# Optimization experiments

Hardware: AMD Instinct MI355X
Metric: run time of the kernel (lower is better)

## Reference

```python
import jax, jax.numpy as jnp
import numpy as np

# Dims (match init_kwargs): d_model=1024, H=16 heads, hd=64, lift=2 -> Nlift=128, top-k t=32
B, T, D = 1, 2048, 1024
H, HD, LIFT, TK = 16, 64, 2, 32
N = LIFT * HD  # 128 lifted dims per head
EPS = 1e-12


def topk_sparsify(x, k):
    """ReLU then keep only the top-k values per last-dim row (rest zeroed).
    Mathematically identical to the torch COO top-k construction: the sparse
    matrix equals the dense matrix with non-top-k entries zeroed."""
    x = jax.nn.relu(x)
    vals, idx = jax.lax.top_k(x, k)              # (..., k)
    n = x.shape[-1]
    flat_idx = idx.reshape(-1, k)
    flat_vals = vals.reshape(-1, k)
    R = flat_idx.shape[0]
    out = jnp.zeros((R, n), dtype=x.dtype)
    out = out.at[jnp.arange(R)[:, None], flat_idx].set(flat_vals)
    return out.reshape(x.shape)


def setup_inputs() -> dict:
    key = jax.random.key(0)
    ks = jax.random.split(key, 6)
    x = jax.random.normal(ks[0], (B, T, D), jnp.float32)
    W_q = jax.random.normal(ks[1], (H * N, D), jnp.float32) * 0.02
    W_k = jax.random.normal(ks[2], (H * N, D), jnp.float32) * 0.02
    W_v = jax.random.normal(ks[3], (H * HD, D), jnp.float32) * 0.02
    W_o = jax.random.normal(ks[4], (D, H * HD), jnp.float32) * 0.02
    sink = jax.random.normal(ks[5], (H, HD), jnp.float32) * 0.02
    log_beta = jnp.zeros((), jnp.float32)
    return {"x": x, "W_q": W_q, "W_k": W_k, "W_v": W_v, "W_o": W_o,
            "sink": sink, "log_beta": log_beta}


def reference(x, W_q, W_k, W_v, W_o, sink, log_beta):
    # Projections (Linear with no bias: x @ W.T)
    q = (x @ W_q.T).reshape(B, T, H, N)
    k = (x @ W_k.T).reshape(B, T, H, N)
    v = (x @ W_v.T).reshape(B, T, H, HD)

    # ReLU + top-k sparsification of lifted Q/K rows
    qs = topk_sparsify(q, TK).transpose(0, 2, 1, 3)  # (B,H,T,N)
    kk = topk_sparsify(k, TK).transpose(0, 2, 1, 3)  # (B,H,T,N)

    # A = Qs @ Ks^T per (batch, head) block; spspmm only produces same-block
    # entries, so the per-head batched matmul is the exact dense equivalent.
    A = jnp.einsum('bhin,bhjn->bhij', qs, kk)        # (B,H,T,T), all >= 0

    # Causal filter: keep j <= i
    causal = jnp.tril(jnp.ones((T, T), dtype=bool))
    A = jnp.where(causal, A, jnp.zeros((), A.dtype))

    # p=1 normalization with learned sink mass beta
    denom = A.sum(-1)                                # (B,H,T)
    beta = jnp.exp(log_beta)
    denom_ws = denom + beta
    A = A / jnp.maximum(denom_ws, EPS)[..., None]

    vh = v.transpose(0, 2, 1, 3)                     # (B,H,T,HD)
    Y = jnp.einsum('bhij,bhjd->bhid', A, vh)         # (B,H,T,HD)
    Y = Y + (beta / denom_ws)[..., None] * sink[None, :, None, :]

    Y = Y.transpose(0, 2, 1, 3).reshape(B, T, H * HD)
    return Y @ W_o.T
```

## Files before the change

### kernel.cpp

```cpp
#include <hip/hip_runtime.h>

typedef __attribute__((ext_vector_type(8))) short bf8v;
typedef __attribute__((ext_vector_type(4))) float f4v;
typedef unsigned short u16;
typedef unsigned int   u32;
#define AS1 __attribute__((address_space(1)))
#define AS3 __attribute__((address_space(3)))

__device__ inline u16 f2b(float f){
  u32 u = __builtin_bit_cast(u32, f);
  u += 0x7fffu + ((u >> 16) & 1u);
  return (u16)(u >> 16);
}

__global__ __launch_bounds__(256) void conv_all(const float* __restrict__ x,  const float* __restrict__ wq,
                                                const float* __restrict__ wk, const float* __restrict__ wv,
                                                const float* __restrict__ wo,
                                                u16* xb, u16* wqb, u16* wkb, u16* wvb, u16* wob){
  int i = blockIdx.x * 256 + threadIdx.x;
  const float* src; u16* dst; int off;
  if      (i <  524288){ src = x;  dst = xb;  off = i; }
  else if (i < 1048576){ src = wq; dst = wqb; off = i -  524288; }
  else if (i < 1572864){ src = wk; dst = wkb; off = i - 1048576; }
  else if (i < 1835008){ src = wv; dst = wvb; off = i - 1572864; }
  else                 { src = wo; dst = wob; off = i - 1835008; }
  float4 v = ((const float4*)src)[off];
  uint2 r;
  r.x = (u32)f2b(v.x) | ((u32)f2b(v.y) << 16);
  r.y = (u32)f2b(v.z) | ((u32)f2b(v.w) << 16);
  ((uint2*)dst)[off] = r;
}

template<int NFR>
__device__ __forceinline__ void gemm_core(const u16* __restrict__ A, const u16* __restrict__ B,
                                          int K, int m0, int n0, u16* lds, f4v (&acc)[4][NFR]){
  const int tid = threadIdx.x;
  const int l = tid & 63, w = tid >> 6;
  const int wrow = (w >> 1) * 64, wcol = (w & 1) * (NFR * 16);
  constexpr int SB = 8192 + NFR * 2048;
  #pragma unroll
  for (int a = 0; a < 4; a++)
    #pragma unroll
    for (int b = 0; b < NFR; b++) acc[a][b] = (f4v)0.0f;

  const int crow = l >> 3;
  const int ksrc = ((l & 7) ^ crow) * 8;

  auto stage = [&](int k0, int buf){
    const u16* Ab = A + (size_t)m0 * K + k0;
    const u16* Bb = B + (size_t)n0 * K + k0;
    u16* At = lds + buf * SB;
    u16* Bt = At + 8192;
    #pragma unroll
    for (int c = 0; c < 4; c++){
      int chunk = w * 4 + c;
      int row = chunk * 8 + crow;
      __builtin_amdgcn_global_load_lds((const AS1 void*)(Ab + (size_t)row * K + ksrc),
                                       (AS3 void*)(At + chunk * 512), 16, 0, 0);
    }
    if constexpr (NFR == 4){
      #pragma unroll
      for (int c = 0; c < 4; c++){
        int chunk = w * 4 + c;
        int row = chunk * 8 + crow;
        __builtin_amdgcn_global_load_lds((const AS1 void*)(Bb + (size_t)row * K + ksrc),
                                         (AS3 void*)(Bt + chunk * 512), 16, 0, 0);
      }
    } else {
      #pragma unroll
      for (int c = 0; c < 2; c++){
        int chunk = w * 2 + c;
        int row = chunk * 8 + crow;
        __builtin_amdgcn_global_load_lds((const AS1 void*)(Bb + (size_t)row * K + ksrc),
                                         (AS3 void*)(Bt + chunk * 512), 16, 0, 0);
      }
    }
  };

  stage(0, 0);
  __syncthreads();
  int buf = 0;
  for (int k0 = 0; k0 < K; k0 += 64){
    if (k0 + 64 < K) stage(k0 + 64, buf ^ 1);
    const u16* At = lds + buf * SB;
    const u16* Bt = At + 8192;
    #pragma unroll
    for (int kk = 0; kk < 2; kk++){
      bf8v af[4], bfr[NFR];
      #pragma unroll
      for (int mr = 0; mr < 4; mr++){
        int row = wrow + mr * 16 + (l & 15);
        af[mr] = *(const bf8v*)(At + row * 64 + (((kk * 32 + (l >> 4) * 8)) ^ ((row & 7) * 8)));
      }
      #pragma unroll
      for (int nc = 0; nc < NFR; nc++){
        int row = wcol + nc * 16 + (l & 15);
        bfr[nc] = *(const bf8v*)(Bt + row * 64 + (((kk * 32 + (l >> 4) * 8)) ^ ((row & 7) * 8)));
      }
      #pragma unroll
      for (int mr = 0; mr < 4; mr++)
        #pragma unroll
        for (int nc = 0; nc < NFR; nc++)
          acc[mr][nc] = __builtin_amdgcn_mfma_f32_16x16x32_bf16(af[mr], bfr[nc], acc[mr][nc], 0, 0, 0);
    }
    __syncthreads();
    buf ^= 1;
  }
}

__global__ __launch_bounds__(256) void qkv_gemm(const u16* __restrict__ xb,
                                                const u16* __restrict__ wqb, const u16* __restrict__ wkb,
                                                const u16* __restrict__ wvb,
                                                u16* qf, u16* kf, u16* vtb){
  __shared__ u16 lds[32768];
  int b = (blockIdx.x & 7) * 80 + (blockIdx.x >> 3);
  const u16* Bp; int which;
  if (b < 256)      { Bp = wqb; which = 0; }
  else if (b < 512) { Bp = wkb; which = 1; b -= 256; }
  else              { Bp = wvb; which = 2; b -= 512; }
  int sh = (which == 2) ? 3 : 4;
  int m0 = (b >> sh) * 128, n0 = (b & ((1 << sh) - 1)) * 128;

  f4v acc[4][4];
  gemm_core<4>(xb, Bp, 1024, m0, n0, lds, acc);

  const int l = threadIdx.x & 63, w = threadIdx.x >> 6;
  const int wrow = (w >> 1) * 64, wcol = (w & 1) * 64;
  if (which < 2){
    u16* C = which ? kf : qf;
    #pragma unroll
    for (int mr = 0; mr < 4; mr++)
      #pragma unroll
      for (int nc = 0; nc < 4; nc++)
        #pragma unroll
        for (int rr = 0; rr < 4; rr++){
          int row = m0 + wrow + mr * 16 + (l >> 4) * 4 + rr;
          int col = n0 + wcol + nc * 16 + (l & 15);
          C[(size_t)row * 2048 + col] = f2b(acc[mr][nc][rr]);
        }
  } else {
    #pragma unroll
    for (int mr = 0; mr < 4; mr++)
      #pragma unroll
      for (int nc = 0; nc < 4; nc++){
        int gcol = n0 + wcol + nc * 16 + (l & 15);
        int t0 = m0 + wrow + mr * 16 + (l >> 4) * 4;
        uint2 pk;
        pk.x = (u32)f2b(acc[mr][nc][0]) | ((u32)f2b(acc[mr][nc][1]) << 16);
        pk.y = (u32)f2b(acc[mr][nc][2]) | ((u32)f2b(acc[mr][nc][3]) << 16);
        *(uint2*)(vtb + (size_t)gcol * 2048 + t0) = pk;
      }
  }
}

__global__ __launch_bounds__(256) void o_gemm(const u16* __restrict__ yb, const u16* __restrict__ wob,
                                              float* out){
  __shared__ u16 lds[24576];
  int b = (blockIdx.x & 7) * 32 + (blockIdx.x >> 3);
  int m0 = (b >> 4) * 128, n0 = (b & 15) * 64;
  f4v acc[4][2];
  gemm_core<2>(yb, wob, 1024, m0, n0, lds, acc);
  const int l = threadIdx.x & 63, w = threadIdx.x >> 6;
  const int wrow = (w >> 1) * 64, wcol = (w & 1) * 32;
  #pragma unroll
  for (int mr = 0; mr < 4; mr++)
    #pragma unroll
    for (int nc = 0; nc < 2; nc++)
      #pragma unroll
      for (int rr = 0; rr < 4; rr++){
        int row = m0 + wrow + mr * 16 + (l >> 4) * 4 + rr;
        int col = n0 + wcol + nc * 16 + (l & 15);
        out[(size_t)row * 1024 + col] = acc[mr][nc][rr];
      }
}

__global__ __launch_bounds__(256) void topk2(const u16* __restrict__ qf, const u16* __restrict__ kf,
                                             u16* __restrict__ qsb, u16* __restrict__ ksb){
  int w = threadIdx.x >> 6, l = threadIdx.x & 63;
  int b = blockIdx.x;
  const u16* src; u16* dst;
  if (b < 2048){ src = qf; dst = qsb; } else { src = kf; dst = ksb; b -= 2048; }
  int base = b * 16 + w * 4;
  u32 u0[4], u1[4], pre[4];
  int tt[4], hh[4];
  #pragma unroll
  for (int j = 0; j < 4; j++){
    int r = base + j;
    tt[j] = r >> 4; hh[j] = r & 15;
    u32 pair = ((const u32*)(src + (size_t)tt[j] * 2048 + hh[j] * 128))[l];
    u0[j] = pair & 0xFFFFu; u1[j] = pair >> 16;
    if (u0[j] & 0x8000u) u0[j] = 0;
    if (u1[j] & 0x8000u) u1[j] = 0;
    pre[j] = 0;
  }
  for (int bb = 14; bb >= 0; --bb){
    #pragma unroll
    for (int j = 0; j < 4; j++){
      u32 cand = pre[j] | (1u << bb);
      int c = __builtin_popcountll(__ballot(u0[j] >= cand)) + __builtin_popcountll(__ballot(u1[j] >= cand));
      if (c >= 32) pre[j] = cand;
    }
  }
  #pragma unroll
  for (int j = 0; j < 4; j++){
    u32 o0 = (u0[j] >= pre[j]) ? u0[j] : 0u;
    u32 o1 = (u1[j] >= pre[j]) ? u1[j] : 0u;
    ((u32*)(dst + ((size_t)hh[j] * 2048 + tt[j]) * 128))[l] = o0 | (o1 << 16);
  }
}

__global__ __launch_bounds__(512) void attn3(const u16* __restrict__ qs, const u16* __restrict__ ks,
                                             const u16* __restrict__ vt, const float* __restrict__ sink,
                                             const float* __restrict__ logbeta, u16* __restrict__ yout,
                                             float* __restrict__ Yp, float* __restrict__ Dp){
  __shared__ u16 Kt[2][8192];
  __shared__ u16 Vt[2][4096];
  __shared__ u16 St[8][16 * 72];
  const int tid = threadIdx.x, l = tid & 63, w = tid >> 6;
  const int b = blockIdx.x;
  const int slot = b >> 3;
  const int h = (b & 7) + 8 * (slot / 40);
  const int u = slot % 40;
  int it, chunk, nch;
  if (u < 4)       { it = u; chunk = 0; nch = 1; }
  else if (u < 12) { it = 4 + ((u - 4) >> 1);  chunk = (u - 4) & 1;  nch = 2; }
  else if (u < 24) { it = 8 + (u - 12) / 3;    chunk = (u - 12) % 3; nch = 3; }
  else             { it = 12 + ((u - 24) >> 2); chunk = (u - 24) & 3; nch = 4; }
  const int tiles = 2 * it + 2;
  const int jt0 = (tiles * chunk) / nch;
  const int jt1 = (tiles * (chunk + 1)) / nch;
  const int qrow0 = it * 128 + w * 16;
  const float beta = expf(logbeta[0]);

  bf8v qfr[4];
  {
    int trow = qrow0 + (l & 15);
    const u16* qrow = qs + ((size_t)h * 2048 + trow) * 128 + (l >> 4) * 8;
    #pragma unroll
    for (int kk = 0; kk < 4; kk++) qfr[kk] = *(const bf8v*)(qrow + kk * 32);
  }

  f4v accY[4];
  #pragma unroll
  for (int c = 0; c < 4; c++) accY[c] = (f4v)0.0f;
  float dsum[4] = {0.f, 0.f, 0.f, 0.f};

  const u16* kroot = ks + (size_t)h * 2048 * 128;
  const u16* vroot = vt + (size_t)h * 64 * 2048;

  auto stage = [&](int jt, int buf){
    const u16* kbase = kroot + (size_t)jt * 64 * 128;
    #pragma unroll
    for (int i = 0; i < 2; i++){
      int g = i * 512 + tid;
      int r = g >> 4, c = g & 15;
      __builtin_amdgcn_global_load_lds((const AS1 void*)(kbase + r * 128 + (c ^ (r & 7)) * 8),
                                       (AS3 void*)(&Kt[buf][(i * 512 + w * 64) * 8]), 16, 0, 0);
    }
    {
      int d = tid >> 3, c = tid & 7;
      __builtin_amdgcn_global_load_lds((const AS1 void*)(vroot + (size_t)d * 2048 + jt * 64 + (c ^ (d & 7)) * 8),
                                       (AS3 void*)(&Vt[buf][w * 512]), 16, 0, 0);
    }
  };

  stage(jt0, 0);
  __syncthreads();
  int buf = 0;
  for (int jt = jt0; jt < jt1; ++jt){
    if (jt + 1 < jt1) stage(jt + 1, buf ^ 1);

    if (jt * 64 <= qrow0 + 15){
      f4v accS[4];
      #pragma unroll
      for (int c = 0; c < 4; c++) accS[c] = (f4v)0.0f;
      __builtin_amdgcn_s_setprio(1);
      #pragma unroll
      for (int c = 0; c < 4; c++){
        int r = c * 16 + (l & 15);
        #pragma unroll
        for (int kk = 0; kk < 4; kk++){
          int ch = kk * 4 + (l >> 4);
          bf8v kfr = *(const bf8v*)(&Kt[buf][r * 128 + ((ch ^ (r & 7)) * 8)]);
          accS[c] = __builtin_amdgcn_mfma_f32_16x16x32_bf16(qfr[kk], kfr, accS[c], 0, 0, 0);
        }
      }
      __builtin_amdgcn_s_setprio(0);
      if (jt * 64 + 63 > qrow0){
        #pragma unroll
        for (int c = 0; c < 4; c++)
          #pragma unroll
          for (int rr = 0; rr < 4; rr++){
            int i = qrow0 + (l >> 4) * 4 + rr;
            int j = jt * 64 + c * 16 + (l & 15);
            if (j > i) accS[c][rr] = 0.f;
          }
      }
      #pragma unroll
      for (int c = 0; c < 4; c++)
        #pragma unroll
        for (int rr = 0; rr < 4; rr++){
          dsum[rr] += accS[c][rr];
          St[w][((l >> 4) * 4 + rr) * 72 + c * 16 + (l & 15)] = f2b(accS[c][rr]);
        }
      __builtin_amdgcn_s_setprio(1);
      #pragma unroll
      for (int k2 = 0; k2 < 2; k2++){
        bf8v afr = *(const bf8v*)(&St[w][(l & 15) * 72 + k2 * 32 + (l >> 4) * 8]);
        #pragma unroll
        for (int c = 0; c < 4; c++){
          int d = c * 16 + (l & 15);
          int ch = k2 * 4 + (l >> 4);
          bf8v vfr = *(const bf8v*)(&Vt[buf][d * 64 + ((ch ^ (d & 7)) * 8)]);
          accY[c] = __builtin_amdgcn_mfma_f32_16x16x32_bf16(afr, vfr, accY[c], 0, 0, 0);
        }
      }
      __builtin_amdgcn_s_setprio(0);
    }
    __syncthreads();
    buf ^= 1;
  }

  #pragma unroll
  for (int rr = 0; rr < 4; rr++){
    float s = dsum[rr];
    s += __shfl_xor(s, 1, 64);
    s += __shfl_xor(s, 2, 64);
    s += __shfl_xor(s, 4, 64);
    s += __shfl_xor(s, 8, 64);
    dsum[rr] = s;
  }

  if (nch == 1){
    #pragma unroll
    for (int c = 0; c < 4; c++){
      float sv = sink[h * 64 + c * 16 + (l & 15)];
      #pragma unroll
      for (int rr = 0; rr < 4; rr++){
        float den = dsum[rr] + beta;
        float inv = 1.0f / fmaxf(den, 1e-12f);
        float y = (accY[c][rr] + beta * sv) * inv;
        int row = qrow0 + (l >> 4) * 4 + rr;
        yout[(size_t)row * 1024 + h * 64 + c * 16 + (l & 15)] = f2b(y);
      }
    }
  } else {
    float* yp = Yp + ((size_t)h * 40 + u) * 8192;
    #pragma unroll
    for (int c = 0; c < 4; c++)
      #pragma unroll
      for (int rr = 0; rr < 4; rr++){
        int rowib = w * 16 + (l >> 4) * 4 + rr;
        yp[rowib * 64 + c * 16 + (l & 15)] = accY[c][rr];
      }
    if ((l & 15) == 0){
      #pragma unroll
      for (int rr = 0; rr < 4; rr++)
        Dp[((size_t)h * 40 + u) * 128 + w * 16 + (l >> 4) * 4 + rr] = dsum[rr];
    }
  }
}

__global__ __launch_bounds__(256) void attn_reduce(const float* __restrict__ Yp, const float* __restrict__ Dp,
                                                   const float* __restrict__ sink, const float* __restrict__ logbeta,
                                                   u16* __restrict__ yout){
  int blk = blockIdx.x;
  int h = blk / 12, it = 4 + blk % 12;
  int nch = it / 4 + 1;
  int u0 = (it < 8) ? 4 + (it - 4) * 2 : (it < 12) ? 12 + (it - 8) * 3 : 24 + (it - 12) * 4;
  float beta = expf(logbeta[0]);
  __shared__ float inv_s[128];
  int t = threadIdx.x;
  if (t < 128){
    float s = 0.f;
    for (int c = 0; c < nch; c++) s += Dp[((size_t)h * 40 + u0 + c) * 128 + t];
    inv_s[t] = 1.0f / fmaxf(s + beta, 1e-12f);
  }
  __syncthreads();
  const float* base = Yp + ((size_t)h * 40 + u0) * 8192;
  #pragma unroll
  for (int e = 0; e < 32; e++){
    int idx = e * 256 + t;
    float acc = 0.f;
    for (int c = 0; c < nch; c++) acc += base[c * 8192 + idx];
    int row = idx >> 6, col = idx & 63;
    float y = (acc + beta * sink[h * 64 + col]) * inv_s[row];
    yout[(size_t)(it * 128 + row) * 1024 + h * 64 + col] = f2b(y);
  }
}

extern "C" void kernel_launch(void* const* d_in, const int* in_sizes, int n_in,
                              void* d_out, int out_size, void* d_ws, size_t ws_size,
                              hipStream_t stream){
  const float* x    = (const float*)d_in[0];
  const float* Wq   = (const float*)d_in[1];
  const float* Wk   = (const float*)d_in[2];
  const float* Wv   = (const float*)d_in[3];
  const float* Wo   = (const float*)d_in[4];
  const float* sink = (const float*)d_in[5];
  const float* logb = (const float*)d_in[6];

  char* ws = (char*)d_ws;
  u16*   xb  = (u16*)(ws + 0);
  u16*   wqb = (u16*)(ws + 4194304);
  u16*   wkb = (u16*)(ws + 8388608);
  u16*   wvb = (u16*)(ws + 12582912);
  u16*   wob = (u16*)(ws + 14680064);
  u16*   qf  = (u16*)(ws + 16777216);
  u16*   kf  = (u16*)(ws + 33554432);
  u16*   qsb = (u16*)(ws + 50331648);
  u16*   ksb = (u16*)(ws + 58720256);
  u16*   vtb = (u16*)(ws + 67108864);
  u16*   yb  = (u16*)(ws + 71303168);
  float* Yp  = (float*)(ws + 16777216);
  float* Dp  = (float*)(ws + 37748736);

  conv_all<<<8192, 256, 0, stream>>>(x, Wq, Wk, Wv, Wo, xb, wqb, wkb, wvb, wob);
  qkv_gemm<<<640, 256, 0, stream>>>(xb, wqb, wkb, wvb, qf, kf, vtb);
  topk2<<<4096, 256, 0, stream>>>(qf, kf, qsb, ksb);
  attn3<<<640, 512, 0, stream>>>(qsb, ksb, vtb, sink, logb, yb, Yp, Dp);
  attn_reduce<<<192, 256, 0, stream>>>(Yp, Dp, sink, logb, yb);
  o_gemm<<<256, 256, 0, stream>>>(yb, wob, (float*)d_out);
}
```

Baseline: 140.7 us.

## Shrink GEMM K-tile and single-buffer attention K to raise occupancy

The shared GEMM core now stages 32-wide K slices instead of 64, with a new XOR swizzle, which halves LDS per block. qkv_gemm and o_gemm gain launch-bounds occupancy hints. The attention kernel keeps K in a single LDS buffer, prefetched after a mid-iteration barrier once the S = QK^T MMAs are done, while V stays double-buffered. The goal is more resident blocks per CU to hide latency, at the cost of twice as many K-loop iterations and barriers in the GEMMs and less overlap for K loads in attention.

```diff
diff --git a/kernel.cpp b/kernel.cpp
--- a/kernel.cpp
+++ b/kernel.cpp
@@ -37,82 +37,69 @@
   const int tid = threadIdx.x;
   const int l = tid & 63, w = tid >> 6;
   const int wrow = (w >> 1) * 64, wcol = (w & 1) * (NFR * 16);
-  constexpr int SB = 8192 + NFR * 2048;
+  constexpr int SB = 4096 + NFR * 1024;
   #pragma unroll
   for (int a = 0; a < 4; a++)
     #pragma unroll
     for (int b = 0; b < NFR; b++) acc[a][b] = (f4v)0.0f;
 
-  const int crow = l >> 3;
-  const int ksrc = ((l & 7) ^ crow) * 8;
+  const int lrow = l >> 2;
+  const int lseg = l & 3;
 
   auto stage = [&](int k0, int buf){
-    const u16* Ab = A + (size_t)m0 * K + k0;
-    const u16* Bb = B + (size_t)n0 * K + k0;
     u16* At = lds + buf * SB;
-    u16* Bt = At + 8192;
-    #pragma unroll
-    for (int c = 0; c < 4; c++){
-      int chunk = w * 4 + c;
-      int row = chunk * 8 + crow;
-      __builtin_amdgcn_global_load_lds((const AS1 void*)(Ab + (size_t)row * K + ksrc),
-                                       (AS3 void*)(At + chunk * 512), 16, 0, 0);
-    }
-    if constexpr (NFR == 4){
-      #pragma unroll
-      for (int c = 0; c < 4; c++){
-        int chunk = w * 4 + c;
-        int row = chunk * 8 + crow;
-        __builtin_amdgcn_global_load_lds((const AS1 void*)(Bb + (size_t)row * K + ksrc),
-                                         (AS3 void*)(Bt + chunk * 512), 16, 0, 0);
-      }
-    } else {
-      #pragma unroll
-      for (int c = 0; c < 2; c++){
-        int chunk = w * 2 + c;
-        int row = chunk * 8 + crow;
-        __builtin_amdgcn_global_load_lds((const AS1 void*)(Bb + (size_t)row * K + ksrc),
-                                         (AS3 void*)(Bt + chunk * 512), 16, 0, 0);
-      }
+    u16* Bt = At + 4096;
+    #pragma unroll
+    for (int j = 0; j < 2; j++){
+      int ca = w * 2 + j;
+      int row = ca * 16 + lrow;
+      int sseg = (lseg ^ ((row >> 1) & 3)) * 8;
+      __builtin_amdgcn_global_load_lds((const AS1 void*)(A + (size_t)(m0 + row) * K + k0 + sseg),
+                                       (AS3 void*)(At + ca * 512), 16, 0, 0);
+    }
+    #pragma unroll
+    for (int j = 0; j < NFR / 2; j++){
+      int cb = w * (NFR / 2) + j;
+      int row = cb * 16 + lrow;
+      int sseg = (lseg ^ ((row >> 1) & 3)) * 8;
+      __builtin_amdgcn_global_load_lds((const AS1 void*)(B + (size_t)(n0 + row) * K + k0 + sseg),
+                                       (AS3 void*)(Bt + cb * 512), 16, 0, 0);
     }
   };
 
   stage(0, 0);
   __syncthreads();
   int buf = 0;
-  for (int k0 = 0; k0 < K; k0 += 64){
-    if (k0 + 64 < K) stage(k0 + 64, buf ^ 1);
+  for (int k0 = 0; k0 < K; k0 += 32){
+    if (k0 + 32 < K) stage(k0 + 32, buf ^ 1);
     const u16* At = lds + buf * SB;
-    const u16* Bt = At + 8192;
-    #pragma unroll
-    for (int kk = 0; kk < 2; kk++){
-      bf8v af[4], bfr[NFR];
-      #pragma unroll
-      for (int mr = 0; mr < 4; mr++){
-        int row = wrow + mr * 16 + (l & 15);
-        af[mr] = *(const bf8v*)(At + row * 64 + (((kk * 32 + (l >> 4) * 8)) ^ ((row & 7) * 8)));
-      }
-      #pragma unroll
-      for (int nc = 0; nc < NFR; nc++){
-        int row = wcol + nc * 16 + (l & 15);
-        bfr[nc] = *(const bf8v*)(Bt + row * 64 + (((kk * 32 + (l >> 4) * 8)) ^ ((row & 7) * 8)));
-      }
-      #pragma unroll
-      for (int mr = 0; mr < 4; mr++)
-        #pragma unroll
-        for (int nc = 0; nc < NFR; nc++)
-          acc[mr][nc] = __builtin_amdgcn_mfma_f32_16x16x32_bf16(af[mr], bfr[nc], acc[mr][nc], 0, 0, 0);
-    }
+    const u16* Bt = At + 4096;
+    bf8v af[4], bfr[NFR];
+    #pragma unroll
+    for (int mr = 0; mr < 4; mr++){
+      int row = wrow + mr * 16 + (l & 15);
+      af[mr] = *(const bf8v*)(At + row * 32 + (((l >> 4) ^ ((row >> 1) & 3)) * 8));
+    }
+    #pragma unroll
+    for (int nc = 0; nc < NFR; nc++){
+      int row = wcol + nc * 16 + (l & 15);
+      bfr[nc] = *(const bf8v*)(Bt + row * 32 + (((l >> 4) ^ ((row >> 1) & 3)) * 8));
+    }
+    #pragma unroll
+    for (int mr = 0; mr < 4; mr++)
+      #pragma unroll
+      for (int nc = 0; nc < NFR; nc++)
+        acc[mr][nc] = __builtin_amdgcn_mfma_f32_16x16x32_bf16(af[mr], bfr[nc], acc[mr][nc], 0, 0, 0);
     __syncthreads();
     buf ^= 1;
   }
 }
 
-__global__ __launch_bounds__(256) void qkv_gemm(const u16* __restrict__ xb,
-                                                const u16* __restrict__ wqb, const u16* __restrict__ wkb,
-                                                const u16* __restrict__ wvb,
-                                                u16* qf, u16* kf, u16* vtb){
-  __shared__ u16 lds[32768];
+__global__ __launch_bounds__(256, 4) void qkv_gemm(const u16* __restrict__ xb,
+                                                   const u16* __restrict__ wqb, const u16* __restrict__ wkb,
+                                                   const u16* __restrict__ wvb,
+                                                   u16* qf, u16* kf, u16* vtb){
+  __shared__ u16 lds[16384];
   int b = (blockIdx.x & 7) * 80 + (blockIdx.x >> 3);
   const u16* Bp; int which;
   if (b < 256)      { Bp = wqb; which = 0; }
@@ -153,9 +140,9 @@
   }
 }
 
-__global__ __launch_bounds__(256) void o_gemm(const u16* __restrict__ yb, const u16* __restrict__ wob,
-                                              float* out){
-  __shared__ u16 lds[24576];
+__global__ __launch_bounds__(256, 4) void o_gemm(const u16* __restrict__ yb, const u16* __restrict__ wob,
+                                                 float* out){
+  __shared__ u16 lds[12288];
   int b = (blockIdx.x & 7) * 32 + (blockIdx.x >> 3);
   int m0 = (b >> 4) * 128, n0 = (b & 15) * 64;
   f4v acc[4][2];
@@ -209,11 +196,11 @@
   }
 }
 
-__global__ __launch_bounds__(512) void attn3(const u16* __restrict__ qs, const u16* __restrict__ ks,
-                                             const u16* __restrict__ vt, const float* __restrict__ sink,
-                                             const float* __restrict__ logbeta, u16* __restrict__ yout,
-                                             float* __restrict__ Yp, float* __restrict__ Dp){
-  __shared__ u16 Kt[2][8192];
+__global__ __launch_bounds__(512, 6) void attn3(const u16* __restrict__ qs, const u16* __restrict__ ks,
+                                                const u16* __restrict__ vt, const float* __restrict__ sink,
+                                                const float* __restrict__ logbeta, u16* __restrict__ yout,
+                                                float* __restrict__ Yp, float* __restrict__ Dp){
+  __shared__ u16 Kt[8192];
   __shared__ u16 Vt[2][4096];
   __shared__ u16 St[8][16 * 72];
   const int tid = threadIdx.x, l = tid & 63, w = tid >> 6;
@@ -248,30 +235,33 @@
   const u16* kroot = ks + (size_t)h * 2048 * 128;
   const u16* vroot = vt + (size_t)h * 64 * 2048;
 
-  auto stage = [&](int jt, int buf){
+  auto stageK = [&](int jt){
     const u16* kbase = kroot + (size_t)jt * 64 * 128;
     #pragma unroll
     for (int i = 0; i < 2; i++){
       int g = i * 512 + tid;
       int r = g >> 4, c = g & 15;
       __builtin_amdgcn_global_load_lds((const AS1 void*)(kbase + r * 128 + (c ^ (r & 7)) * 8),
-                                       (AS3 void*)(&Kt[buf][(i * 512 + w * 64) * 8]), 16, 0, 0);
-    }
-    {
-      int d = tid >> 3, c = tid & 7;
-      __builtin_amdgcn_global_load_lds((const AS1 void*)(vroot + (size_t)d * 2048 + jt * 64 + (c ^ (d & 7)) * 8),
-                                       (AS3 void*)(&Vt[buf][w * 512]), 16, 0, 0);
+                                       (AS3 void*)(&Kt[(i * 512 + w * 64) * 8]), 16, 0, 0);
     }
   };
-
-  stage(jt0, 0);
+  auto stageV = [&](int jt, int b2){
+    int d = tid >> 3, c = tid & 7;
+    __builtin_amdgcn_global_load_lds((const AS1 void*)(vroot + (size_t)d * 2048 + jt * 64 + (c ^ (d & 7)) * 8),
+                                     (AS3 void*)(&Vt[b2][w * 512]), 16, 0, 0);
+  };
+
+  stageK(jt0);
+  stageV(jt0, 0);
   __syncthreads();
   int buf = 0;
   for (int jt = jt0; jt < jt1; ++jt){
-    if (jt + 1 < jt1) stage(jt + 1, buf ^ 1);
-
-    if (jt * 64 <= qrow0 + 15){
-      f4v accS[4];
+    bool pf = (jt + 1 < jt1);
+    if (pf) stageV(jt + 1, buf ^ 1);
+    const bool act = (jt * 64 <= qrow0 + 15);
+
+    f4v accS[4];
+    if (act){
       #pragma unroll
       for (int c = 0; c < 4; c++) accS[c] = (f4v)0.0f;
       __builtin_amdgcn_s_setprio(1);
@@ -281,11 +271,17 @@
         #pragma unroll
         for (int kk = 0; kk < 4; kk++){
           int ch = kk * 4 + (l >> 4);
-          bf8v kfr = *(const bf8v*)(&Kt[buf][r * 128 + ((ch ^ (r & 7)) * 8)]);
+          bf8v kfr = *(const bf8v*)(&Kt[r * 128 + ((ch ^ (r & 7)) * 8)]);
           accS[c] = __builtin_amdgcn_mfma_f32_16x16x32_bf16(qfr[kk], kfr, accS[c], 0, 0, 0);
         }
       }
       __builtin_amdgcn_s_setprio(0);
+    }
+    __builtin_amdgcn_s_barrier();
+    __builtin_amdgcn_sched_barrier(0);
+    if (pf) stageK(jt + 1);
+
+    if (act){
       if (jt * 64 + 63 > qrow0){
         #pragma unroll
         for (int c = 0; c < 4; c++)
```

Measured after the change: 136.9 us, median of 3. 2.7% less time.
